# Optimization experiments

Measured on AMD Instinct MI355X. Metric: run time of the kernel, lower is better.

The kernel has to match this reference:

```python
import jax, jax.numpy as jnp
import numpy as np

DIM = 2048
N_HEADS = 32
HEAD_DIM = DIM // N_HEADS
D_FF = 4 * DIM
EPS = 1e-5


def layernorm(x, g, b):
    mu = jnp.mean(x, axis=-1, keepdims=True)
    var = jnp.mean(jnp.square(x - mu), axis=-1, keepdims=True)
    return (x - mu) * jax.lax.rsqrt(var + EPS) * g + b


def setup_inputs() -> dict:
    key = jax.random.key(0)
    ks = jax.random.split(key, 12)
    s = 0.02
    # Linear weights stored as [in, out] (y = x @ W + b), equivalent math to torch's x @ W.T
    return {
        "x": jax.random.normal(ks[0], (2, 2048, DIM), jnp.float32),
        "w_qkv": jax.random.normal(ks[1], (DIM, 3 * DIM), jnp.float32) * s,
        "b_qkv": jnp.zeros((3 * DIM,), jnp.float32),
        "w_o": jax.random.normal(ks[2], (DIM, DIM), jnp.float32) * s,
        "b_o": jnp.zeros((DIM,), jnp.float32),
        "g1": jnp.ones((DIM,), jnp.float32),
        "beta1": jnp.zeros((DIM,), jnp.float32),
        "w1": jax.random.normal(ks[3], (DIM, D_FF), jnp.float32) * s,
        "b1": jnp.zeros((D_FF,), jnp.float32),
        "w2": jax.random.normal(ks[4], (D_FF, DIM), jnp.float32) * s,
        "b2": jnp.zeros((DIM,), jnp.float32),
        "g2": jnp.ones((DIM,), jnp.float32),
        "beta2": jnp.zeros((DIM,), jnp.float32),
    }


def reference(x, w_qkv, b_qkv, w_o, b_o, g1, beta1, w1, b1, w2, b2, g2, beta2):
    B, T, _ = x.shape
    residual = x
    h = layernorm(x, g1, beta1)
    qkv = h @ w_qkv + b_qkv                      # [B,T,3*DIM]
    qkv = qkv.reshape(B, T, 3, N_HEADS, HEAD_DIM)
    qkv = jnp.transpose(qkv, (2, 0, 3, 1, 4))    # [3,B,H,T,D]
    q, k, v = qkv[0], qkv[1], qkv[2]
    scores = jnp.einsum("bhtd,bhsd->bhts", q, k) / np.sqrt(HEAD_DIM).astype(np.float32)
    attn = jax.nn.softmax(scores, axis=-1)       # full T x T (non-causal), as in source
    out = jnp.einsum("bhts,bhsd->bhtd", attn, v)
    out = jnp.transpose(out, (0, 2, 1, 3)).reshape(B, T, DIM)
    h = out @ w_o + b_o
    x = h + residual
    residual = x
    h = layernorm(x, g2, beta2)
    h = jax.nn.gelu(h @ w1 + b1, approximate=False)  # torch nn.GELU default = exact erf
    h = h @ w2 + b2
    return h + residual
```

## Files before the change

kernel.cpp:

```cpp
#include <hip/hip_runtime.h>
#include <hip/hip_bf16.h>

#define DIM  2048
#define DFF  8192
#define NH   32
#define HD   64
#define TT   2048
#define MM   4096

typedef __attribute__((ext_vector_type(4))) float f32x4;
typedef __attribute__((ext_vector_type(4))) unsigned int u32x4;
typedef __attribute__((ext_vector_type(2))) unsigned int u32x2;
typedef unsigned short ushort_t;

#define MFMA16(ACC, A, B) \
  asm volatile("v_mfma_f32_16x16x32_bf16 %0, %1, %2, %0" : "+v"(ACC) : "v"(A), "v"(B))

#define GL16(GP, LP)                                                     \
  __builtin_amdgcn_global_load_lds(                                      \
      (const __attribute__((address_space(1))) void*)(GP),               \
      (__attribute__((address_space(3))) void*)(LP), 16, 0, 0)

__device__ __forceinline__ unsigned int f2bu(float f) {
  union { __hip_bfloat16 h; unsigned short u; } c;
  c.h = __float2bfloat16(f);
  return (unsigned int)c.u;
}

__global__ __launch_bounds__(256)
void transpose_cvt(const float* __restrict__ in, __hip_bfloat16* __restrict__ out,
                   int R, int C) {
  __shared__ float tile[32][33];
  const int tx = threadIdx.x, ty = threadIdx.y;
  const int bx = blockIdx.x * 32, by = blockIdx.y * 32;
#pragma unroll
  for (int i = 0; i < 32; i += 8)
    tile[ty + i][tx] = in[(size_t)(by + ty + i) * C + bx + tx];
  __syncthreads();
#pragma unroll
  for (int i = 0; i < 32; i += 8)
    out[(size_t)(bx + ty + i) * R + by + tx] = __float2bfloat16(tile[tx][ty + i]);
}

__global__ __launch_bounds__(256)
void ln_kernel(const float* __restrict__ in, const float* __restrict__ gw,
               const float* __restrict__ bw, __hip_bfloat16* __restrict__ out) {
  const int row = blockIdx.x;
  const int t = threadIdx.x;
  const float* x = in + (size_t)row * DIM;
  const float4 v0 = ((const float4*)x)[t * 2];
  const float4 v1 = ((const float4*)x)[t * 2 + 1];
  float s  = v0.x + v0.y + v0.z + v0.w + v1.x + v1.y + v1.z + v1.w;
  float ss = v0.x*v0.x + v0.y*v0.y + v0.z*v0.z + v0.w*v0.w
           + v1.x*v1.x + v1.y*v1.y + v1.z*v1.z + v1.w*v1.w;
#pragma unroll
  for (int o = 32; o >= 1; o >>= 1) { s += __shfl_xor(s, o); ss += __shfl_xor(ss, o); }
  __shared__ float red[8];
  if ((t & 63) == 0) { red[t >> 6] = s; red[4 + (t >> 6)] = ss; }
  __syncthreads();
  s  = red[0] + red[1] + red[2] + red[3];
  ss = red[4] + red[5] + red[6] + red[7];
  const float mean = s * (1.0f / DIM);
  const float rstd = rsqrtf(ss * (1.0f / DIM) - mean * mean + 1e-5f);
  const float4 g0 = ((const float4*)gw)[t * 2], g1 = ((const float4*)gw)[t * 2 + 1];
  const float4 b0 = ((const float4*)bw)[t * 2], b1 = ((const float4*)bw)[t * 2 + 1];
  uint4 o;
  o.x = f2bu((v0.x - mean) * rstd * g0.x + b0.x) | (f2bu((v0.y - mean) * rstd * g0.y + b0.y) << 16);
  o.y = f2bu((v0.z - mean) * rstd * g0.z + b0.z) | (f2bu((v0.w - mean) * rstd * g0.w + b0.w) << 16);
  o.z = f2bu((v1.x - mean) * rstd * g1.x + b1.x) | (f2bu((v1.y - mean) * rstd * g1.y + b1.y) << 16);
  o.w = f2bu((v1.z - mean) * rstd * g1.z + b1.z) | (f2bu((v1.w - mean) * rstd * g1.w + b1.w) << 16);
  *(uint4*)((char*)out + ((size_t)row * DIM + t * 8) * 2) = o;
}

template <int EPI>
__global__ __launch_bounds__(512, 2)
void gemm256(const __hip_bfloat16* __restrict__ Abf, const __hip_bfloat16* __restrict__ Btbf,
             const float* __restrict__ bias, const float* __restrict__ res,
             void* __restrict__ o0, void* __restrict__ o1, void* __restrict__ o2,
             int M, int N, int K, int nkt) {
  __shared__ ushort_t lds[2][2][16384];
  const int tid = threadIdx.x;
  const int l = tid & 63, w = tid >> 6;
  const int wm = w >> 2, wn = w & 3;
  const int g = l >> 4, q15 = l & 15;

  const int nby = M >> 8;
  const int nwg = (N >> 8) * nby;
  int id = blockIdx.x;
  {
    const int qq = nwg >> 3, rr = nwg & 7;
    const int xcd = id & 7, pos = id >> 3;
    id = (xcd < rr ? xcd * (qq + 1) : rr * (qq + 1) + (xcd - rr) * qq) + pos;
  }
  const int bm = (id % nby) << 8;
  const int bn = (id / nby) << 8;
  const int k0 = (EPI == 4) ? (int)blockIdx.y * (nkt << 6) : 0;

  const ushort_t* Au = (const ushort_t*)Abf;
  const ushort_t* Bu = (const ushort_t*)Btbf;
  const int sr = tid >> 3;
  const int sc = (((tid & 7) ^ (sr & 7)) << 3);
  const ushort_t* aBase = Au + (size_t)(bm + sr) * K + (k0 + sc);
  const ushort_t* bBase = Bu + (size_t)(bn + sr) * K + (k0 + sc);
  const int dOff = (w << 9) + (l << 3);

#define STG(ab, grp, dbuf, kkk)                                          \
  GL16(((ab) ? bBase : aBase) + (size_t)((grp) << 6) * K + (kkk),        \
       &lds[dbuf][ab][((grp) << 12) + dOff])

#define AFRAG(dbuf, m, ks)                                               \
  (*(const u32x4*)&lds[dbuf][0][((((wm) << 7) + ((m) << 4) + q15) << 6) + \
                                (((((ks) << 2) | g) ^ (q15 & 7)) << 3)])
#define BFRAG(dbuf, n, ks)                                               \
  (*(const u32x4*)&lds[dbuf][1][((((wn) << 6) + ((n) << 4) + q15) << 6) + \
                                (((((ks) << 2) | g) ^ (q15 & 7)) << 3)])

  f32x4 acc[8][4];
#pragma unroll
  for (int a = 0; a < 8; ++a)
#pragma unroll
    for (int b = 0; b < 4; ++b) acc[a][b] = (f32x4)0.0f;

  STG(1, 0, 0, 0); STG(1, 1, 0, 0); STG(1, 2, 0, 0); STG(1, 3, 0, 0);
  STG(0, 0, 0, 0); STG(0, 2, 0, 0); STG(0, 1, 0, 0); STG(0, 3, 0, 0);
  asm volatile("s_waitcnt vmcnt(2)" ::: "memory");
  __builtin_amdgcn_s_barrier();

  int cur = 0;
  for (int kt = 0; kt < nkt; ++kt) {
    const int nxt = cur ^ 1;
    const bool hn = (kt + 1) < nkt;
    const int kk = (kt + 1) << 6;
    u32x4 bf[4][2], af[2][2];

    if (hn) { STG(1, 0, nxt, kk); STG(1, 1, nxt, kk); }
#pragma unroll
    for (int n = 0; n < 4; ++n)
#pragma unroll
      for (int ks = 0; ks < 2; ++ks) bf[n][ks] = BFRAG(cur, n, ks);
#pragma unroll
    for (int mm = 0; mm < 2; ++mm)
#pragma unroll
      for (int ks = 0; ks < 2; ++ks) af[mm][ks] = AFRAG(cur, mm, ks);
    __builtin_amdgcn_s_barrier();
    asm volatile("s_waitcnt lgkmcnt(0)" ::: "memory");
    __builtin_amdgcn_s_setprio(1);
#pragma unroll
    for (int ks = 0; ks < 2; ++ks)
#pragma unroll
      for (int mm = 0; mm < 2; ++mm)
#pragma unroll
        for (int n = 0; n < 4; ++n) MFMA16(acc[mm][n], af[mm][ks], bf[n][ks]);
    __builtin_amdgcn_s_setprio(0);
    __builtin_amdgcn_s_barrier();

    if (hn) { STG(1, 2, nxt, kk); STG(1, 3, nxt, kk); }
#pragma unroll
    for (int mm = 0; mm < 2; ++mm)
#pragma unroll
      for (int ks = 0; ks < 2; ++ks) af[mm][ks] = AFRAG(cur, 2 + mm, ks);
    if (hn) asm volatile("s_waitcnt vmcnt(4)" ::: "memory");
    else    asm volatile("s_waitcnt vmcnt(0)" ::: "memory");
    __builtin_amdgcn_s_barrier();
    asm volatile("s_waitcnt lgkmcnt(0)" ::: "memory");
    __builtin_amdgcn_s_setprio(1);
#pragma unroll
    for (int ks = 0; ks < 2; ++ks)
#pragma unroll
      for (int mm = 0; mm < 2; ++mm)
#pragma unroll
        for (int n = 0; n < 4; ++n) MFMA16(acc[2 + mm][n], af[mm][ks], bf[n][ks]);
    __builtin_amdgcn_s_setprio(0);
    __builtin_amdgcn_s_barrier();

    if (hn) { STG(0, 0, nxt, kk); STG(0, 2, nxt, kk); }
#pragma unroll
    for (int mm = 0; mm < 2; ++mm)
#pragma unroll
      for (int ks = 0; ks < 2; ++ks) af[mm][ks] = AFRAG(cur, 4 + mm, ks);
    __builtin_amdgcn_s_barrier();
    asm volatile("s_waitcnt lgkmcnt(0)" ::: "memory");
    __builtin_amdgcn_s_setprio(1);
#pragma unroll
    for (int ks = 0; ks < 2; ++ks)
#pragma unroll
      for (int mm = 0; mm < 2; ++mm)
#pragma unroll
        for (int n = 0; n < 4; ++n) MFMA16(acc[4 + mm][n], af[mm][ks], bf[n][ks]);
    __builtin_amdgcn_s_setprio(0);
    __builtin_amdgcn_s_barrier();

    if (hn) { STG(0, 1, nxt, kk); STG(0, 3, nxt, kk); }
#pragma unroll
    for (int mm = 0; mm < 2; ++mm)
#pragma unroll
      for (int ks = 0; ks < 2; ++ks) af[mm][ks] = AFRAG(cur, 6 + mm, ks);
    if (hn) asm volatile("s_waitcnt vmcnt(2)" ::: "memory");
    __builtin_amdgcn_s_barrier();
    asm volatile("s_waitcnt lgkmcnt(0)" ::: "memory");
    __builtin_amdgcn_s_setprio(1);
#pragma unroll
    for (int ks = 0; ks < 2; ++ks)
#pragma unroll
      for (int mm = 0; mm < 2; ++mm)
#pragma unroll
        for (int n = 0; n < 4; ++n) MFMA16(acc[6 + mm][n], af[mm][ks], bf[n][ks]);
    __builtin_amdgcn_s_setprio(0);
    __builtin_amdgcn_s_barrier();

    cur = nxt;
  }

#pragma unroll
  for (int m = 0; m < 8; ++m) {
    const int row0 = bm + (wm << 7) + (m << 4) + (g << 2);
#pragma unroll
    for (int n = 0; n < 4; ++n) {
      const int col = bn + (wn << 6) + (n << 4) + q15;
      float bv = 0.0f;
      if constexpr (EPI != 4) bv = bias[col];
#pragma unroll
      for (int i = 0; i < 4; ++i) {
        const int mrow = row0 + i;
        float v = acc[m][n][i] + bv;
        if constexpr (EPI == 0) {
          const int sel = col >> 11, hd = col & 2047, h = hd >> 6, d = hd & 63;
          const int b = mrow >> 11, t = mrow & 2047;
          if (sel == 0) {
            ((__hip_bfloat16*)o0)[((size_t)(b * NH + h) * TT + t) * HD + d] =
                __float2bfloat16(v * 0.125f);
          } else if (sel == 1) {
            ((__hip_bfloat16*)o1)[((size_t)(b * NH + h) * TT + t) * HD + d] =
                __float2bfloat16(v);
          } else {
            ((__hip_bfloat16*)o2)[((size_t)(b * NH + h) * HD + d) * TT + t] =
                __float2bfloat16(v);
          }
        } else if constexpr (EPI == 2) {
          ((__hip_bfloat16*)o0)[(size_t)mrow * N + col] =
              __float2bfloat16(0.5f * v * (1.0f + erff(v * 0.70710678118654752f)));
        } else {
          ((float*)(blockIdx.y ? o1 : o0))[(size_t)mrow * N + col] = v;
        }
      }
    }
  }
#undef STG
#undef AFRAG
#undef BFRAG
}

__global__ __launch_bounds__(256)
void combine2(const float* __restrict__ p0, const float* __restrict__ p1,
              const float* __restrict__ bias, const float* __restrict__ res,
              float* __restrict__ out) {
  const size_t i = ((size_t)blockIdx.x * 256 + threadIdx.x) << 2;
  const float4 a = *(const float4*)(p0 + i);
  const float4 b = *(const float4*)(p1 + i);
  const float4 r = *(const float4*)(res + i);
  const float4 bi = *(const float4*)(bias + (i & (DIM - 1)));
  float4 o;
  o.x = a.x + b.x + r.x + bi.x;
  o.y = a.y + b.y + r.y + bi.y;
  o.z = a.z + b.z + r.z + bi.z;
  o.w = a.w + b.w + r.w + bi.w;
  *(float4*)(out + i) = o;
}

template <int EPI>
__global__ __launch_bounds__(256)
void gemm_bt(const __hip_bfloat16* __restrict__ A, const __hip_bfloat16* __restrict__ Bt,
             const float* __restrict__ bias, const float* __restrict__ res,
             void* __restrict__ o0, int M, int N, int K) {
  __shared__ __hip_bfloat16 As[128 * 32];
  __shared__ __hip_bfloat16 Bs[128 * 32];
  const int tid = threadIdx.x;
  const int l = tid & 63, w = tid >> 6;
  const int wr = w >> 1, wc = w & 1;
  const int g = l >> 4, q15 = l & 15;
  const int bm = blockIdx.y * 128, bn = blockIdx.x * 128;

  f32x4 acc[4][4];
#pragma unroll
  for (int a = 0; a < 4; ++a)
#pragma unroll
    for (int b = 0; b < 4; ++b) acc[a][b] = (f32x4)0.0f;

  const __hip_bfloat16* aSrc = A  + (size_t)(bm + (tid >> 2)) * K + (tid & 3) * 8;
  const __hip_bfloat16* bSrc = Bt + (size_t)(bn + (tid >> 2)) * K + (tid & 3) * 8;
  __hip_bfloat16* aDst = As + tid * 8;
  __hip_bfloat16* bDst = Bs + tid * 8;
  const size_t rowStep = (size_t)64 * K;

  for (int kt = 0; kt < K; kt += 32) {
    GL16(aSrc + kt,            aDst);
    GL16(aSrc + rowStep + kt,  aDst + 2048);
    GL16(bSrc + kt,            bDst);
    GL16(bSrc + rowStep + kt,  bDst + 2048);
    __syncthreads();
    u32x4 af[4], bf[4];
#pragma unroll
    for (int rb = 0; rb < 4; ++rb)
      af[rb] = *(const u32x4*)(As + (wr * 64 + rb * 16 + q15) * 32 + g * 8);
#pragma unroll
    for (int cb = 0; cb < 4; ++cb)
      bf[cb] = *(const u32x4*)(Bs + (wc * 64 + cb * 16 + q15) * 32 + g * 8);
#pragma unroll
    for (int rb = 0; rb < 4; ++rb)
#pragma unroll
      for (int cb = 0; cb < 4; ++cb) MFMA16(acc[rb][cb], af[rb], bf[cb]);
    __syncthreads();
  }

#pragma unroll
  for (int rb = 0; rb < 4; ++rb) {
    const int row0 = bm + wr * 64 + rb * 16 + g * 4;
#pragma unroll
    for (int cb = 0; cb < 4; ++cb) {
      const int col = bn + wc * 64 + cb * 16 + q15;
      const float bv = bias[col];
#pragma unroll
      for (int i = 0; i < 4; ++i) {
        const int m = row0 + i;
        float v = acc[rb][cb][i] + bv;
        ((float*)o0)[(size_t)m * N + col] = v + res[(size_t)m * N + col];
      }
    }
  }
}

__global__ __launch_bounds__(256)
void attn_kernel(const __hip_bfloat16* __restrict__ Q, const __hip_bfloat16* __restrict__ Kx,
                 const __hip_bfloat16* __restrict__ Vt, __hip_bfloat16* __restrict__ out) {
  __shared__ unsigned int Plds[4][2048];
  const int tid = threadIdx.x;
  const int l = tid & 63, w = tid >> 6;
  const int g = l >> 4, q15 = l & 15;
  const int bh = blockIdx.x >> 3;
  const int q0 = (blockIdx.x & 7) * 256 + w * 64;
  const __hip_bfloat16* Qb = Q  + (size_t)bh * TT * HD;
  const __hip_bfloat16* Kb = Kx + (size_t)bh * TT * HD;
  const __hip_bfloat16* Vb = Vt + (size_t)bh * HD * TT;
  unsigned int* Pw = Plds[w];

  u32x4 qf[4][2];
#pragma unroll
  for (int rb = 0; rb < 4; ++rb)
#pragma unroll
    for (int ks = 0; ks < 2; ++ks)
      qf[rb][ks] = *(const u32x4*)(Qb + (size_t)(q0 + rb * 16 + q15) * HD + ks * 32 + g * 8);

  f32x4 acc[4][4];
#pragma unroll
  for (int a = 0; a < 4; ++a)
#pragma unroll
    for (int b = 0; b < 4; ++b) acc[a][b] = (f32x4)0.0f;
  float mstat[4] = {-3e38f, -3e38f, -3e38f, -3e38f};
  float lstat[4] = {0.f, 0.f, 0.f, 0.f};

  for (int s0 = 0; s0 < TT; s0 += 64) {
    f32x4 st[4][4];
#pragma unroll
    for (int a = 0; a < 4; ++a)
#pragma unroll
      for (int b = 0; b < 4; ++b) st[a][b] = (f32x4)0.0f;
#pragma unroll
    for (int ks = 0; ks < 2; ++ks) {
      u32x4 kf[4];
#pragma unroll
      for (int cb = 0; cb < 4; ++cb)
        kf[cb] = *(const u32x4*)(Kb + (size_t)(s0 + cb * 16 + q15) * HD + ks * 32 + g * 8);
#pragma unroll
      for (int cb = 0; cb < 4; ++cb)
#pragma unroll
        for (int rb = 0; rb < 4; ++rb) MFMA16(st[cb][rb], kf[cb], qf[rb][ks]);
    }
#pragma unroll
    for (int rb = 0; rb < 4; ++rb) {
      float pm = st[0][rb][0];
#pragma unroll
      for (int cb = 0; cb < 4; ++cb)
#pragma unroll
        for (int i = 0; i < 4; ++i) pm = fmaxf(pm, st[cb][rb][i]);
      pm = fmaxf(pm, __shfl_xor(pm, 16));
      pm = fmaxf(pm, __shfl_xor(pm, 32));
      const float mnew = fmaxf(mstat[rb], pm);
      const float corr = __expf(mstat[rb] - mnew);
      mstat[rb] = mnew;
      float rs = 0.f;
#pragma unroll
      for (int cb = 0; cb < 4; ++cb)
#pragma unroll
        for (int i = 0; i < 4; ++i) {
          const float p = __expf(st[cb][rb][i] - mnew);
          st[cb][rb][i] = p;
          rs += p;
        }
      rs += __shfl_xor(rs, 16);
      rs += __shfl_xor(rs, 32);
      lstat[rb] = lstat[rb] * corr + rs;
#pragma unroll
      for (int db = 0; db < 4; ++db)
#pragma unroll
        for (int i = 0; i < 4; ++i) acc[db][rb][i] *= corr;
      const int row = rb * 16 + q15;
      const int rx = row & 7;
#pragma unroll
      for (int cb = 0; cb < 4; ++cb) {
        const unsigned int lo = f2bu(st[cb][rb][0]) | (f2bu(st[cb][rb][1]) << 16);
        const unsigned int hi = f2bu(st[cb][rb][2]) | (f2bu(st[cb][rb][3]) << 16);
        const int seg = (cb * 2 + (g >> 1)) ^ rx;
        u32x2 pk = {lo, hi};
        *(u32x2*)(Pw + row * 32 + seg * 4 + (g & 1) * 2) = pk;
      }
    }
#pragma unroll
    for (int ks2 = 0; ks2 < 2; ++ks2) {
      u32x4 vf[4], pf[4];
#pragma unroll
      for (int db = 0; db < 4; ++db)
        vf[db] = *(const u32x4*)(Vb + (size_t)(db * 16 + q15) * TT + s0 + ks2 * 32 + g * 8);
#pragma unroll
      for (int rb = 0; rb < 4; ++rb) {
        const int row = rb * 16 + q15;
        const int seg = (ks2 * 4 + g) ^ (row & 7);
        pf[rb] = *(const u32x4*)(Pw + row * 32 + seg * 4);
      }
#pragma unroll
      for (int db = 0; db < 4; ++db)
#pragma unroll
        for (int rb = 0; rb < 4; ++rb) MFMA16(acc[db][rb], vf[db], pf[rb]);
    }
  }
  const int b = bh >> 5, hh = bh & 31;
#pragma unroll
  for (int rb = 0; rb < 4; ++rb) {
    const float inv = 1.0f / lstat[rb];
    const size_t trow = (size_t)(b * TT + q0 + rb * 16 + q15);
#pragma unroll
    for (int db = 0; db < 4; ++db) {
      const unsigned int lo = f2bu(acc[db][rb][0] * inv) | (f2bu(acc[db][rb][1] * inv) << 16);
      const unsigned int hi = f2bu(acc[db][rb][2] * inv) | (f2bu(acc[db][rb][3] * inv) << 16);
      u32x2 pk = {lo, hi};
      *(u32x2*)(out + trow * DIM + hh * 64 + db * 16 + g * 4) = pk;
    }
  }
}

extern "C" void kernel_launch(void* const* d_in, const int* in_sizes, int n_in,
                              void* d_out, int out_size, void* d_ws, size_t ws_size,
                              hipStream_t stream) {
  (void)in_sizes; (void)n_in; (void)out_size; (void)ws_size;
  const float* x     = (const float*)d_in[0];
  const float* w_qkv = (const float*)d_in[1];
  const float* b_qkv = (const float*)d_in[2];
  const float* w_o   = (const float*)d_in[3];
  const float* b_o   = (const float*)d_in[4];
  const float* g1    = (const float*)d_in[5];
  const float* be1   = (const float*)d_in[6];
  const float* w1    = (const float*)d_in[7];
  const float* b1    = (const float*)d_in[8];
  const float* w2    = (const float*)d_in[9];
  const float* b2    = (const float*)d_in[10];
  const float* g2    = (const float*)d_in[11];
  const float* be2   = (const float*)d_in[12];

  char* ws = (char*)d_ws;
  size_t off = 0;
  auto alloc = [&](size_t bytes) {
    void* p = ws + off;
    off += (bytes + 255) & ~(size_t)255;
    return p;
  };
  __hip_bfloat16* WqkvT = (__hip_bfloat16*)alloc((size_t)6144 * 2048 * 2);
  __hip_bfloat16* WoT   = (__hip_bfloat16*)alloc((size_t)2048 * 2048 * 2);
  __hip_bfloat16* W1T   = (__hip_bfloat16*)alloc((size_t)8192 * 2048 * 2);
  __hip_bfloat16* W2T   = (__hip_bfloat16*)alloc((size_t)2048 * 8192 * 2);
  __hip_bfloat16* hbuf  = (__hip_bfloat16*)alloc((size_t)MM * DIM * 2);
  float*          xres  = (float*)alloc((size_t)MM * DIM * 4);
  __hip_bfloat16* Qb    = (__hip_bfloat16*)alloc((size_t)MM * DIM * 2);
  __hip_bfloat16* Kb    = (__hip_bfloat16*)alloc((size_t)MM * DIM * 2);
  __hip_bfloat16* Vtb   = (__hip_bfloat16*)alloc((size_t)MM * DIM * 2);
  __hip_bfloat16* attno = (__hip_bfloat16*)alloc((size_t)MM * DIM * 2);
  __hip_bfloat16* f1    = Qb;
  float* p0 = (float*)ws;
  float* p1 = (float*)(ws + (size_t)MM * DIM * 4);

  const dim3 tb(32, 8);
  transpose_cvt<<<dim3(6144 / 32, 2048 / 32), tb, 0, stream>>>(w_qkv, WqkvT, 2048, 6144);
  transpose_cvt<<<dim3(2048 / 32, 2048 / 32), tb, 0, stream>>>(w_o, WoT, 2048, 2048);
  transpose_cvt<<<dim3(8192 / 32, 2048 / 32), tb, 0, stream>>>(w1, W1T, 2048, 8192);
  transpose_cvt<<<dim3(2048 / 32, 8192 / 32), tb, 0, stream>>>(w2, W2T, 8192, 2048);

  ln_kernel<<<MM, 256, 0, stream>>>(x, g1, be1, hbuf);
  gemm256<0><<<dim3((6144 / 256) * (MM / 256)), 512, 0, stream>>>(
      hbuf, WqkvT, b_qkv, nullptr, Qb, Kb, Vtb, MM, 6144, 2048, 32);
  attn_kernel<<<512, 256, 0, stream>>>(Qb, Kb, Vtb, attno);
  gemm_bt<1><<<dim3(2048 / 128, MM / 128), 256, 0, stream>>>(
      attno, WoT, b_o, x, xres, MM, 2048, 2048);
  ln_kernel<<<MM, 256, 0, stream>>>(xres, g2, be2, hbuf);
  gemm256<2><<<dim3((8192 / 256) * (MM / 256)), 512, 0, stream>>>(
      hbuf, W1T, b1, nullptr, f1, nullptr, nullptr, MM, 8192, 2048, 32);
  gemm256<4><<<dim3((2048 / 256) * (MM / 256), 2), 512, 0, stream>>>(
      f1, W2T, nullptr, nullptr, p0, p1, nullptr, MM, 2048, 8192, 64);
  combine2<<<(MM * DIM) / 1024, 256, 0, stream>>>(p0, p1, b2, xres, (float*)d_out);
}
```

Baseline: 766.3 us.

## Deepen GEMM global-to-LDS prefetch to two k-tiles ahead with remapped warp rows

The bf16 GEMM main loop now issues global-to-LDS loads up to two k-tiles ahead instead of one, overlapping the two LDS buffers by refilling sub-groups of the current buffer once their fragments have been read. The wait counts and barriers are restructured to match, and the per-wave A-row mapping is interleaved (m&4 selects the upper 128 rows) so each A sub-group is consumed earlier and can be overwritten sooner. The aim is to hide more global memory latency behind MFMA work. The fragile vmcnt bookkeeping risks races or stalls if the counts are wrong.

```diff
diff --git a/kernel.cpp b/kernel.cpp
--- a/kernel.cpp
+++ b/kernel.cpp
@@ -104,16 +104,20 @@
   const ushort_t* bBase = Bu + (size_t)(bn + sr) * K + (k0 + sc);
   const int dOff = (w << 9) + (l << 3);
 
-#define STG(ab, grp, dbuf, kkk)                                          \
-  GL16(((ab) ? bBase : aBase) + (size_t)((grp) << 6) * K + (kkk),        \
-       &lds[dbuf][ab][((grp) << 12) + dOff])
-
-#define AFRAG(dbuf, m, ks)                                               \
-  (*(const u32x4*)&lds[dbuf][0][((((wm) << 7) + ((m) << 4) + q15) << 6) + \
-                                (((((ks) << 2) | g) ^ (q15 & 7)) << 3)])
-#define BFRAG(dbuf, n, ks)                                               \
-  (*(const u32x4*)&lds[dbuf][1][((((wn) << 6) + ((n) << 4) + q15) << 6) + \
-                                (((((ks) << 2) | g) ^ (q15 & 7)) << 3)])
+#define SA(buf, grp, kt_)                                                \
+  GL16(aBase + (size_t)((grp) << 6) * K + ((kt_) << 6),                  \
+       &lds[buf][0][((grp) << 12) + dOff])
+#define SB(buf, grp, kt_)                                                \
+  GL16(bBase + (size_t)((grp) << 6) * K + ((kt_) << 6),                  \
+       &lds[buf][1][((grp) << 12) + dOff])
+
+#define AFR(buf, m, ks)                                                        \
+  (*(const u32x4*)&lds[buf][0][(((((m) & 4) << 5) + (wm << 6) +                \
+                                 (((m) & 3) << 4) + q15) << 6) +               \
+                               (((((ks) << 2) | g) ^ (q15 & 7)) << 3)])
+#define BFR(buf, n, ks)                                                        \
+  (*(const u32x4*)&lds[buf][1][((((wn) << 6) + ((n) << 4) + q15) << 6) +       \
+                               (((((ks) << 2) | g) ^ (q15 & 7)) << 3)])
 
   f32x4 acc[8][4];
 #pragma unroll
@@ -121,27 +125,27 @@
 #pragma unroll
     for (int b = 0; b < 4; ++b) acc[a][b] = (f32x4)0.0f;
 
-  STG(1, 0, 0, 0); STG(1, 1, 0, 0); STG(1, 2, 0, 0); STG(1, 3, 0, 0);
-  STG(0, 0, 0, 0); STG(0, 2, 0, 0); STG(0, 1, 0, 0); STG(0, 3, 0, 0);
-  asm volatile("s_waitcnt vmcnt(2)" ::: "memory");
+  SB(0, 0, 0); SB(0, 1, 0); SB(0, 2, 0); SB(0, 3, 0);
+  SA(0, 0, 0); SA(0, 1, 0); SA(0, 2, 0); SA(0, 3, 0);
+  SB(1, 0, 1); SB(1, 1, 1); SB(1, 2, 1); SB(1, 3, 1);
+  SA(1, 0, 1); SA(1, 1, 1);
+  asm volatile("s_waitcnt vmcnt(8)" ::: "memory");
   __builtin_amdgcn_s_barrier();
 
-  int cur = 0;
   for (int kt = 0; kt < nkt; ++kt) {
-    const int nxt = cur ^ 1;
-    const bool hn = (kt + 1) < nkt;
-    const int kk = (kt + 1) << 6;
+    const int cur = kt & 1, oth = cur ^ 1;
+    const bool p1 = (kt + 1) < nkt, p2 = (kt + 2) < nkt;
     u32x4 bf[4][2], af[2][2];
 
-    if (hn) { STG(1, 0, nxt, kk); STG(1, 1, nxt, kk); }
+    if (p1) { SA(oth, 2, kt + 1); SA(oth, 3, kt + 1); }
 #pragma unroll
     for (int n = 0; n < 4; ++n)
 #pragma unroll
-      for (int ks = 0; ks < 2; ++ks) bf[n][ks] = BFRAG(cur, n, ks);
+      for (int ks = 0; ks < 2; ++ks) bf[n][ks] = BFR(cur, n, ks);
 #pragma unroll
     for (int mm = 0; mm < 2; ++mm)
 #pragma unroll
-      for (int ks = 0; ks < 2; ++ks) af[mm][ks] = AFRAG(cur, mm, ks);
+      for (int ks = 0; ks < 2; ++ks) af[mm][ks] = AFR(cur, mm, ks);
     __builtin_amdgcn_s_barrier();
     asm volatile("s_waitcnt lgkmcnt(0)" ::: "memory");
     __builtin_amdgcn_s_setprio(1);
@@ -154,13 +158,11 @@
     __builtin_amdgcn_s_setprio(0);
     __builtin_amdgcn_s_barrier();
 
-    if (hn) { STG(1, 2, nxt, kk); STG(1, 3, nxt, kk); }
+    if (p2) { SB(cur, 0, kt + 2); SB(cur, 1, kt + 2); }
 #pragma unroll
     for (int mm = 0; mm < 2; ++mm)
 #pragma unroll
-      for (int ks = 0; ks < 2; ++ks) af[mm][ks] = AFRAG(cur, 2 + mm, ks);
-    if (hn) asm volatile("s_waitcnt vmcnt(4)" ::: "memory");
-    else    asm volatile("s_waitcnt vmcnt(0)" ::: "memory");
+      for (int ks = 0; ks < 2; ++ks) af[mm][ks] = AFR(cur, 2 + mm, ks);
     __builtin_amdgcn_s_barrier();
     asm volatile("s_waitcnt lgkmcnt(0)" ::: "memory");
     __builtin_amdgcn_s_setprio(1);
@@ -171,13 +173,16 @@
 #pragma unroll
         for (int n = 0; n < 4; ++n) MFMA16(acc[2 + mm][n], af[mm][ks], bf[n][ks]);
     __builtin_amdgcn_s_setprio(0);
-    __builtin_amdgcn_s_barrier();
-
-    if (hn) { STG(0, 0, nxt, kk); STG(0, 2, nxt, kk); }
+    if (p2)      asm volatile("s_waitcnt vmcnt(10)" ::: "memory");
+    else if (p1) asm volatile("s_waitcnt vmcnt(8)"  ::: "memory");
+    else         asm volatile("s_waitcnt vmcnt(0)"  ::: "memory");
+    __builtin_amdgcn_s_barrier();
+
+    if (p2) { SB(cur, 2, kt + 2); SB(cur, 3, kt + 2); }
 #pragma unroll
     for (int mm = 0; mm < 2; ++mm)
 #pragma unroll
-      for (int ks = 0; ks < 2; ++ks) af[mm][ks] = AFRAG(cur, 4 + mm, ks);
+      for (int ks = 0; ks < 2; ++ks) af[mm][ks] = AFR(cur, 4 + mm, ks);
     __builtin_amdgcn_s_barrier();
     asm volatile("s_waitcnt lgkmcnt(0)" ::: "memory");
     __builtin_amdgcn_s_setprio(1);
@@ -190,12 +195,11 @@
     __builtin_amdgcn_s_setprio(0);
     __builtin_amdgcn_s_barrier();
 
-    if (hn) { STG(0, 1, nxt, kk); STG(0, 3, nxt, kk); }
+    if (p2) { SA(cur, 0, kt + 2); SA(cur, 1, kt + 2); }
 #pragma unroll
     for (int mm = 0; mm < 2; ++mm)
 #pragma unroll
-      for (int ks = 0; ks < 2; ++ks) af[mm][ks] = AFRAG(cur, 6 + mm, ks);
-    if (hn) asm volatile("s_waitcnt vmcnt(2)" ::: "memory");
+      for (int ks = 0; ks < 2; ++ks) af[mm][ks] = AFR(cur, 6 + mm, ks);
     __builtin_amdgcn_s_barrier();
     asm volatile("s_waitcnt lgkmcnt(0)" ::: "memory");
     __builtin_amdgcn_s_setprio(1);
@@ -206,14 +210,14 @@
 #pragma unroll
         for (int n = 0; n < 4; ++n) MFMA16(acc[6 + mm][n], af[mm][ks], bf[n][ks]);
     __builtin_amdgcn_s_setprio(0);
-    __builtin_amdgcn_s_barrier();
-
-    cur = nxt;
+    if (p2)      asm volatile("s_waitcnt vmcnt(8)" ::: "memory");
+    else if (p1) asm volatile("s_waitcnt vmcnt(2)" ::: "memory");
+    __builtin_amdgcn_s_barrier();
   }
 
 #pragma unroll
   for (int m = 0; m < 8; ++m) {
-    const int row0 = bm + (wm << 7) + (m << 4) + (g << 2);
+    const int row0 = bm + ((m & 4) << 5) + (wm << 6) + ((m & 3) << 4) + (g << 2);
 #pragma unroll
     for (int n = 0; n < 4; ++n) {
       const int col = bn + (wn << 6) + (n << 4) + q15;
@@ -245,9 +249,10 @@
       }
     }
   }
-#undef STG
-#undef AFRAG
-#undef BFRAG
+#undef SA
+#undef SB
+#undef AFR
+#undef BFR
 }
 
 __global__ __launch_bounds__(256)
```

After: 772.9 us. No clear change (+0.9%).
